# Performance work log

Measured on AMD Instinct MI355X. Metric: run time of the kernel, lower is better.

Reference implementation:

```python
import jax, jax.numpy as jnp
import numpy as np

N_NODES = 50000
N_EDGES = 600000
IN_DIM = 128
EDGE_DIM = 64
OUT_DIM = 128
AVG_D_LOG = 2.5
EPS = 1e-5  # std epsilon used by PNA aggregate_std
POST_IN = (4 * 3 + 1) * IN_DIM  # (n_aggr*n_scalers + 1) * in_dim = 1664


def setup_inputs() -> dict:
    key = jax.random.key(0)
    ks = jax.random.split(key, 10)
    node_feat = jax.random.normal(ks[0], (N_NODES, IN_DIM), dtype=jnp.float32)
    edge_feat = jax.random.normal(ks[1], (N_EDGES, EDGE_DIM), dtype=jnp.float32)
    src = jax.random.randint(ks[2], (N_EDGES,), 0, N_NODES, dtype=jnp.int32)
    dst = jax.random.randint(ks[3], (N_EDGES,), 0, N_NODES, dtype=jnp.int32)
    pre_in = 2 * IN_DIM + EDGE_DIM  # 320
    W_pre = jax.random.normal(ks[4], (pre_in, IN_DIM), dtype=jnp.float32) / np.sqrt(pre_in)
    b_pre = jnp.zeros((IN_DIM,), dtype=jnp.float32)
    W_post1 = jax.random.normal(ks[5], (POST_IN, OUT_DIM), dtype=jnp.float32) / np.sqrt(POST_IN)
    b_post1 = jnp.zeros((OUT_DIM,), dtype=jnp.float32)
    W_post2 = jax.random.normal(ks[6], (OUT_DIM, OUT_DIM), dtype=jnp.float32) / np.sqrt(OUT_DIM)
    b_post2 = jnp.zeros((OUT_DIM,), dtype=jnp.float32)
    return {"node_feat": node_feat, "edge_feat": edge_feat, "src": src, "dst": dst,
            "W_pre": W_pre, "b_pre": b_pre, "W_post1": W_post1, "b_post1": b_post1,
            "W_post2": W_post2, "b_post2": b_post2}


def reference(node_feat, edge_feat, src, dst, W_pre, b_pre, W_post1, b_post1, W_post2, b_post2):
    N = node_feat.shape[0]
    # pretrans_edges: concat(src feat, dst feat, edge feat) -> MLP (1 layer + relu)
    z2 = jnp.concatenate([node_feat[src], node_feat[dst], edge_feat], axis=-1)  # [E, 320]
    e = jax.nn.relu(z2 @ W_pre + b_pre)  # [E, in_dim] edge messages

    # segmented multi-aggregator reduce at destination nodes
    deg = jax.ops.segment_sum(jnp.ones((e.shape[0],), e.dtype), dst, num_segments=N)  # [N]
    safe_deg = jnp.maximum(deg, 1.0)[:, None]
    s = jax.ops.segment_sum(e, dst, num_segments=N)
    mean = s / safe_deg
    mean_sq = jax.ops.segment_sum(e * e, dst, num_segments=N) / safe_deg
    var = jax.nn.relu(mean_sq - mean * mean)
    std = jnp.sqrt(var + EPS)
    mx = jax.ops.segment_max(e, dst, num_segments=N)
    mn = jax.ops.segment_min(e, dst, num_segments=N)
    has_edges = (deg > 0)[:, None]
    mean = jnp.where(has_edges, mean, 0.0)
    mx = jnp.where(has_edges, mx, 0.0)
    mn = jnp.where(has_edges, mn, 0.0)
    std = jnp.where(has_edges, std, 0.0)
    agg = jnp.concatenate([mean, mx, mn, std], axis=-1)  # [N, 4*in_dim]

    # scalers: identity, amplification, attenuation
    logd = jnp.log(deg + 1.0)[:, None]
    amp = agg * (logd / AVG_D_LOG)
    att = agg * jnp.where(deg[:, None] > 0, AVG_D_LOG / jnp.maximum(logd, EPS), 0.0)
    h_agg = jnp.concatenate([agg, amp, att], axis=-1)  # [N, 12*in_dim]

    # posttrans: concat(h, aggregated) -> 2-layer MLP, then residual
    h = jnp.concatenate([node_feat, h_agg], axis=-1)  # [N, 13*in_dim]
    h = jax.nn.relu(h @ W_post1 + b_post1)
    h = h @ W_post2 + b_post2
    return h + node_feat  # residual (in_dim == out_dim)
```

## Files before the change

kernel.cpp:

```cpp
#include <hip/hip_runtime.h>
#include <hip/hip_bf16.h>
#include <math.h>

#define N_NODES 50000
#define N_EDGES 600000
#define EG 3750
#define SCAN_NB 196

typedef __attribute__((ext_vector_type(8))) short short8v;
typedef __attribute__((ext_vector_type(4))) short short4v;
typedef __attribute__((ext_vector_type(4))) float f32x4;
typedef __attribute__((ext_vector_type(4))) float float4v;

#define FLT_BIG 3.402823466e38f

__device__ __forceinline__ short f2bf(float f) {
  unsigned int u = __float_as_uint(f);
  u = (u + 0x7FFFu + ((u >> 16) & 1u)) >> 16;
  return (short)u;
}
__device__ __forceinline__ float bf2f(unsigned short s) {
  return __uint_as_float(((unsigned int)s) << 16);
}

__global__ void conv_w_kernel(const float* __restrict__ Wpre, const float* __restrict__ Wp1,
                              const float* __restrict__ Wp2, short* __restrict__ WuvT,
                              short* __restrict__ WeT, short* __restrict__ Wp1T,
                              short* __restrict__ Wp2T, int* __restrict__ deg) {
  int idx = blockIdx.x * 256 + threadIdx.x;
  if (idx < 50048) deg[idx] = 0;
  if (idx < 32768) {
    int c = idx >> 7, k = idx & 127;
    WuvT[idx] = f2bf(Wpre[(k + ((c >> 7) << 7)) * 128 + (c & 127)]);
  } else if (idx < 40960) {
    int o = idx - 32768, n = o >> 6, k = o & 63;
    WeT[o] = f2bf(Wpre[(256 + k) * 128 + n]);
  } else if (idx < 253952) {
    int o = idx - 40960, n = o / 1664, k = o % 1664;
    Wp1T[o] = f2bf(Wp1[k * 128 + n]);
  } else if (idx < 270336) {
    int o = idx - 253952, n = o >> 7, k = o & 127;
    Wp2T[o] = f2bf(Wp2[k * 128 + n]);
  }
}

__global__ void deg_kernel(const int* __restrict__ dst, int* __restrict__ deg) {
  int i = blockIdx.x * blockDim.x + threadIdx.x;
  int stride = gridDim.x * blockDim.x;
  for (; i < N_EDGES; i += stride) atomicAdd(deg + dst[i], 1);
}

__global__ __launch_bounds__(256) void scan1_kernel(const int* __restrict__ deg,
                                                    int* __restrict__ blockSums) {
  __shared__ int red[256];
  int b = blockIdx.x, t = threadIdx.x;
  int n = b * 256 + t;
  red[t] = (n < N_NODES) ? deg[n] : 0;
  __syncthreads();
  for (int off = 128; off > 0; off >>= 1) {
    if (t < off) red[t] += red[t + off];
    __syncthreads();
  }
  if (t == 0) blockSums[b] = red[0];
}

__global__ __launch_bounds__(256) void scan2_kernel(const int* __restrict__ blockSums,
                                                    int* __restrict__ blockOffs) {
  __shared__ int sh[256];
  int t = threadIdx.x;
  int v = (t < SCAN_NB) ? blockSums[t] : 0;
  sh[t] = v;
  __syncthreads();
  for (int off = 1; off < 256; off <<= 1) {
    int u = (t >= off) ? sh[t - off] : 0;
    __syncthreads();
    sh[t] += u;
    __syncthreads();
  }
  if (t < SCAN_NB) blockOffs[t] = sh[t] - v;
}

__global__ __launch_bounds__(256) void scan3_kernel(const int* __restrict__ deg,
                                                    const int* __restrict__ blockOffs,
                                                    int* __restrict__ cursor,
                                                    int* __restrict__ rowStart) {
  __shared__ int sh[256];
  int b = blockIdx.x, t = threadIdx.x;
  int n = b * 256 + t;
  int v = (n < N_NODES) ? deg[n] : 0;
  sh[t] = v;
  __syncthreads();
  for (int off = 1; off < 256; off <<= 1) {
    int u = (t >= off) ? sh[t - off] : 0;
    __syncthreads();
    sh[t] += u;
    __syncthreads();
  }
  int ex = blockOffs[b] + sh[t] - v;
  if (n < N_NODES) { cursor[n] = ex; rowStart[n] = ex; }
  if (n == N_NODES) rowStart[N_NODES] = N_EDGES;
}

__global__ void scatter_kernel(const int* __restrict__ src, const int* __restrict__ dst,
                               int* __restrict__ cursor, const int* __restrict__ rowStart,
                               int4* __restrict__ eid, int* __restrict__ blockA) {
  int i0 = blockIdx.x * blockDim.x + threadIdx.x;
  int stride = gridDim.x * blockDim.x;
  for (int i = i0; i < N_EDGES; i += stride) {
    int d = dst[i];
    int pos = atomicAdd(cursor + d, 1);
    eid[pos] = make_int4(i, src[i], d, 0);
  }
  for (int j = N_EDGES + i0; j < N_EDGES + 64; j += stride)
    eid[j] = make_int4(0, 0, 0, 0);
  for (int b = i0; b <= EG; b += stride) {
    int tgt = (int)((long)b * N_EDGES / EG);
    int lo = 0, hi = N_NODES;
    while (lo < hi) { int mid = (lo + hi) >> 1; if (rowStart[mid] < tgt) lo = mid + 1; else hi = mid; }
    blockA[b] = rowStart[lo];
  }
}

__global__ __launch_bounds__(256) void uv_kernel(const float* __restrict__ nf,
                                                 const short* __restrict__ WuvT,
                                                 short* __restrict__ UV) {
  __shared__ short A[64][136];
  int t = threadIdx.x;
  int lane = t & 63, w = t >> 6;
  int r15 = lane & 15, g = lane >> 4;
  int nb = blockIdx.x * 64;

#pragma unroll
  for (int i = 0; i < 8; i++) {
    int u = t + 256 * i, row = u >> 5, q = u & 31;
    int gn = min(nb + row, N_NODES - 1);
    float4v a = *(const float4v*)(nf + (size_t)gn * 128 + q * 4);
    short4v s;
    s[0] = f2bf(a[0]); s[1] = f2bf(a[1]); s[2] = f2bf(a[2]); s[3] = f2bf(a[3]);
    *(short4v*)(&A[row][q * 4]) = s;
  }
  __syncthreads();

  f32x4 acc[4][4];
#pragma unroll
  for (int m = 0; m < 4; m++)
#pragma unroll
    for (int j = 0; j < 4; j++) acc[m][j] = (f32x4){0.f, 0.f, 0.f, 0.f};

#pragma unroll
  for (int ks = 0; ks < 4; ks++) {
    short8v af[4];
#pragma unroll
    for (int m = 0; m < 4; m++) af[m] = *(const short8v*)(&A[m * 16 + r15][ks * 32 + 8 * g]);
#pragma unroll
    for (int j = 0; j < 4; j++) {
      short8v bf = *(const short8v*)(WuvT + (size_t)((4 * w + j) * 16 + r15) * 128 + ks * 32 + 8 * g);
#pragma unroll
      for (int m = 0; m < 4; m++)
        acc[m][j] = __builtin_amdgcn_mfma_f32_16x16x32_bf16(af[m], bf, acc[m][j], 0, 0, 0);
    }
  }

#pragma unroll
  for (int m = 0; m < 4; m++)
#pragma unroll
    for (int j = 0; j < 4; j++)
#pragma unroll
      for (int r = 0; r < 4; r++) {
        int node = nb + m * 16 + 4 * g + r;
        if (node < N_NODES)
          UV[(size_t)node * 256 + (4 * w + j) * 16 + r15] = f2bf(acc[m][j][r]);
      }
}

__global__ __launch_bounds__(256, 6) void edge_kernel(
    const int4* __restrict__ eid, const int* __restrict__ blockA,
    const float* __restrict__ edge_feat, const float* __restrict__ b_pre,
    const short* __restrict__ UV, const short* __restrict__ WeT,
    float* __restrict__ sum, float* __restrict__ sq,
    float* __restrict__ mx, float* __restrict__ mn) {
  __shared__ short A[32][72];
  __shared__ float E[32][132];
  __shared__ int srcL[2][32], dstL[2][32];

  int t = threadIdx.x;
  int lane = t & 63, w = t >> 6;
  int r15 = lane & 15, g = lane >> 4;

  short8v bfr[2][2];
#pragma unroll
  for (int ks = 0; ks < 2; ks++)
#pragma unroll
    for (int j = 0; j < 2; j++)
      bfr[ks][j] = *(const short8v*)(WeT + (size_t)((2 * w + j) * 16 + r15) * 64 + ks * 32 + 8 * g);

  int c = t & 127, half = t >> 7;
  int cd = t & 63, wrow = t >> 6;
  float bp0 = b_pre[2 * cd], bp1 = b_pre[2 * cd + 1];

  const unsigned short* UVu = (const unsigned short*)UV;
  int A0 = blockA[blockIdx.x], A1 = blockA[blockIdx.x + 1];
  if (A0 >= A1) return;

  float4v ge[2];
  auto LOADE = [&](int e0c) {
#pragma unroll
    for (int i = 0; i < 2; i++) {
      int u = t + 256 * i, e = u >> 4, q = u & 15;
      int pe = eid[min(e0c + e, N_EDGES + 63)].x;
      ge[i] = *(const float4v*)(edge_feat + (size_t)pe * 64 + q * 4);
    }
  };
  auto WRITE_A = [&]() {
#pragma unroll
    for (int i = 0; i < 2; i++) {
      int u = t + 256 * i, e = u >> 4, q = u & 15;
      short4v s4;
      s4[0] = f2bf(ge[i][0]); s4[1] = f2bf(ge[i][1]);
      s4[2] = f2bf(ge[i][2]); s4[3] = f2bf(ge[i][3]);
      *(short4v*)(&A[e][q * 4]) = s4;
    }
  };
  int nsrc = 0, ndst = 0;
  auto IDXLOAD = [&](int e0c) {
    if (t < 32) {
      int4 v = eid[min(e0c + t, N_EDGES + 63)];
      nsrc = v.y; ndst = v.z;
    }
  };

  LOADE(A0);
  IDXLOAD(A0);
  if (t < 32) { srcL[0][t] = nsrc; dstL[0][t] = ndst; }
  WRITE_A();
  IDXLOAD(A0 + 32);
  __syncthreads();

  float a0 = (half == 0) ? 0.f : -FLT_BIG;
  float a1 = (half == 0) ? 0.f : FLT_BIG;
  int prevd = -1;

  int p = 0;
  for (int e0 = A0; e0 < A1; e0 += 32) {
    int cnt = min(32, A1 - e0);
    unsigned int upf[8], vpf[8];
#pragma unroll
    for (int i = 0; i < 8; i++) {
      int rr = min(wrow + 4 * i, cnt - 1);
      int sr = srcL[p][rr], dr = dstL[p][rr];
      upf[i] = *(const unsigned int*)(UVu + (size_t)sr * 256 + 2 * cd);
      vpf[i] = *(const unsigned int*)(UVu + (size_t)dr * 256 + 128 + 2 * cd);
    }
    LOADE(e0 + 32);

    f32x4 acc[2][2];
#pragma unroll
    for (int m = 0; m < 2; m++)
#pragma unroll
      for (int j = 0; j < 2; j++) acc[m][j] = (f32x4){0.f, 0.f, 0.f, 0.f};
#pragma unroll
    for (int m = 0; m < 2; m++)
#pragma unroll
      for (int ks = 0; ks < 2; ks++) {
        short8v af = *(const short8v*)(&A[m * 16 + r15][ks * 32 + 8 * g]);
        acc[m][0] = __builtin_amdgcn_mfma_f32_16x16x32_bf16(af, bfr[ks][0], acc[m][0], 0, 0, 0);
        acc[m][1] = __builtin_amdgcn_mfma_f32_16x16x32_bf16(af, bfr[ks][1], acc[m][1], 0, 0, 0);
      }
#pragma unroll
    for (int m = 0; m < 2; m++)
#pragma unroll
      for (int j = 0; j < 2; j++)
#pragma unroll
        for (int r = 0; r < 4; r++)
          E[m * 16 + 4 * g + r][(2 * w + j) * 16 + r15] = acc[m][j][r];
    __syncthreads();

#pragma unroll
    for (int i = 0; i < 8; i++) {
      int r = wrow + 4 * i;
      float u0 = bf2f((unsigned short)(upf[i] & 0xFFFFu));
      float u1 = bf2f((unsigned short)(upf[i] >> 16));
      float v0 = bf2f((unsigned short)(vpf[i] & 0xFFFFu));
      float v1 = bf2f((unsigned short)(vpf[i] >> 16));
      E[r][2 * cd] = fmaxf(u0 + v0 + E[r][2 * cd] + bp0, 0.f);
      E[r][2 * cd + 1] = fmaxf(u1 + v1 + E[r][2 * cd + 1] + bp1, 0.f);
    }
    __syncthreads();

    {
      int l = lane & 31;
      int dl_ = dstL[p][l];
      int dp_ = (l == 0) ? prevd : dstL[p][l - 1];
      unsigned int bm = (unsigned int)__ballot(dl_ != dp_);
#pragma unroll
      for (int r = 0; r < 32; r++) {
        if (r < cnt) {
          if ((bm >> r) & 1u) {
            int tgt = (r == 0) ? prevd : dstL[p][r - 1];
            if (tgt >= 0) {
              size_t o = (size_t)tgt * 128 + c;
              if (half == 0) { sum[o] = a0; sq[o] = a1; }
              else { mx[o] = a0; mn[o] = a1; }
            }
            if (half == 0) { a0 = 0.f; a1 = 0.f; }
            else { a0 = -FLT_BIG; a1 = FLT_BIG; }
          }
          float e = E[r][c];
          if (half == 0) { a0 += e; a1 += e * e; }
          else { a0 = fmaxf(a0, e); a1 = fminf(a1, e); }
        }
      }
      prevd = dstL[p][cnt - 1];
    }
    WRITE_A();
    if (t < 32) { srcL[p ^ 1][t] = nsrc; dstL[p ^ 1][t] = ndst; }
    IDXLOAD(e0 + 64);
    __syncthreads();
    p ^= 1;
  }
  if (prevd >= 0) {
    size_t o = (size_t)prevd * 128 + c;
    if (half == 0) { sum[o] = a0; sq[o] = a1; }
    else { mx[o] = a0; mn[o] = a1; }
  }
}

__global__ __launch_bounds__(512, 4) void post_kernel(
    const float* __restrict__ node_feat, const int* __restrict__ deg,
    const float* __restrict__ sum, const float* __restrict__ sq,
    const float* __restrict__ mxp, const float* __restrict__ mnp,
    const short* __restrict__ Wp1T, const short* __restrict__ Wp2T,
    const float* __restrict__ b1, const float* __restrict__ b2,
    float* __restrict__ out) {
  __shared__ short Ab[2][64][64];
  __shared__ short T[64][136];
  __shared__ float scalL[64][4];
  int t = threadIdx.x;
  int lane = t & 63, w = t >> 6;
  int r15 = lane & 15, g = lane >> 4;
  int nb = blockIdx.x * 64;

  if (t < 64) {
    int n = min(nb + t, N_NODES - 1);
    float dg = (float)deg[n];
    scalL[t][0] = 1.f / fmaxf(dg, 1.f);
    float logd = logf(dg + 1.f);
    scalL[t][1] = logd * 0.4f;
    scalL[t][2] = (dg > 0.f) ? 2.5f / fmaxf(logd, 1e-5f) : 0.f;
    scalL[t][3] = (dg > 0.f) ? 1.f : 0.f;
  }
  float bb1v = b1[w * 16 + r15];

  int srow = t >> 3, s8 = t & 7;
  int sgn = min(nb + srow, N_NODES - 1);
  float4v ra, rb, qa, qb;

  auto PRE = [&](int c) {
    if (c < 2) {
      const float* np = node_feat + (size_t)sgn * 128 + c * 64 + s8 * 8;
      ra = *(const float4v*)np;
      rb = *(const float4v*)(np + 4);
    } else {
      size_t o = (size_t)sgn * 128 + (c & 1) * 64 + s8 * 8;
      int si = (c - 2) >> 1;
      if (si == 0) { ra = *(const float4v*)(sum + o); rb = *(const float4v*)(sum + o + 4); }
      else if (si == 1) { ra = *(const float4v*)(mxp + o); rb = *(const float4v*)(mxp + o + 4); }
      else if (si == 2) { ra = *(const float4v*)(mnp + o); rb = *(const float4v*)(mnp + o + 4); }
      else {
        ra = *(const float4v*)(sum + o); rb = *(const float4v*)(sum + o + 4);
        qa = *(const float4v*)(sq + o);  qb = *(const float4v*)(sq + o + 4);
      }
    }
  };
  auto WR = [&](int buf, int c) {
    short8v pk;
    if (c < 2) {
#pragma unroll
      for (int r = 0; r < 4; r++) { pk[r] = f2bf(ra[r]); pk[4 + r] = f2bf(rb[r]); }
    } else {
      int si = (c - 2) >> 1;
      float inv = scalL[srow][0];
      bool h = (scalL[srow][3] != 0.f);
      if (si == 0) {
#pragma unroll
        for (int r = 0; r < 4; r++) {
          pk[r] = f2bf(h ? ra[r] * inv : 0.f);
          pk[4 + r] = f2bf(h ? rb[r] * inv : 0.f);
        }
      } else if (si == 1) {
#pragma unroll
        for (int r = 0; r < 4; r++) {
          pk[r] = f2bf(h ? ra[r] : 0.f);
          pk[4 + r] = f2bf(h ? rb[r] : 0.f);
        }
      } else if (si == 2) {
#pragma unroll
        for (int r = 0; r < 4; r++) {
          pk[r] = f2bf(h ? ra[r] : 0.f);
          pk[4 + r] = f2bf(h ? rb[r] : 0.f);
        }
      } else {
#pragma unroll
        for (int r = 0; r < 4; r++) {
          float m0 = ra[r] * inv, m1 = rb[r] * inv;
          float s0 = sqrtf(fmaxf(qa[r] * inv - m0 * m0, 0.f) + 1e-5f);
          float s1 = sqrtf(fmaxf(qb[r] * inv - m1 * m1, 0.f) + 1e-5f);
          pk[r] = f2bf(h ? s0 : 0.f);
          pk[4 + r] = f2bf(h ? s1 : 0.f);
        }
      }
    }
    *(short8v*)(&Ab[buf][0][0] + srow * 64 + (s8 ^ (srow & 7)) * 8) = pk;
  };

  f32x4 accB[4], accC[4], accD[4];
#pragma unroll
  for (int m = 0; m < 4; m++) {
    accB[m] = (f32x4){0.f, 0.f, 0.f, 0.f};
    accC[m] = (f32x4){0.f, 0.f, 0.f, 0.f};
    accD[m] = (f32x4){0.f, 0.f, 0.f, 0.f};
  }

  const short* wrp = Wp1T + (size_t)(w * 16 + r15) * 1664 + 8 * g;

  PRE(0);
  __syncthreads();
  WR(0, 0);
  __syncthreads();

  for (int c = 0; c < 10; c++) {
    int buf = c & 1;
    if (c < 9) PRE(c + 1);
    short8v bw0[3], bw1[3];
    if (c < 2) {
      bw0[0] = *(const short8v*)(wrp + c * 64);
      bw1[0] = *(const short8v*)(wrp + c * 64 + 32);
    } else {
      int ka = (c - 2) * 64;
      bw0[0] = *(const short8v*)(wrp + 128 + ka);
      bw0[1] = *(const short8v*)(wrp + 640 + ka);
      bw0[2] = *(const short8v*)(wrp + 1152 + ka);
      bw1[0] = *(const short8v*)(wrp + 128 + ka + 32);
      bw1[1] = *(const short8v*)(wrp + 640 + ka + 32);
      bw1[2] = *(const short8v*)(wrp + 1152 + ka + 32);
    }
    const short* base = &Ab[buf][0][0];
#pragma unroll
    for (int ks2 = 0; ks2 < 2; ks2++) {
      const short8v* bw = (ks2 == 0) ? bw0 : bw1;
      short8v af[4];
#pragma unroll
      for (int m = 0; m < 4; m++) {
        int row = m * 16 + r15;
        af[m] = *(const short8v*)(base + row * 64 + (((ks2 << 2) | g) ^ (row & 7)) * 8);
      }
      if (c < 2) {
#pragma unroll
        for (int m = 0; m < 4; m++)
          accB[m] = __builtin_amdgcn_mfma_f32_16x16x32_bf16(af[m], bw[0], accB[m], 0, 0, 0);
      } else {
#pragma unroll
        for (int m = 0; m < 4; m++) {
          accB[m] = __builtin_amdgcn_mfma_f32_16x16x32_bf16(af[m], bw[0], accB[m], 0, 0, 0);
          accC[m] = __builtin_amdgcn_mfma_f32_16x16x32_bf16(af[m], bw[1], accC[m], 0, 0, 0);
          accD[m] = __builtin_amdgcn_mfma_f32_16x16x32_bf16(af[m], bw[2], accD[m], 0, 0, 0);
        }
      }
    }
    if (c < 9) WR(buf ^ 1, c + 1);
    __syncthreads();
  }

#pragma unroll
  for (int m = 0; m < 4; m++)
#pragma unroll
    for (int r = 0; r < 4; r++) {
      int row = m * 16 + 4 * g + r;
      float v = accB[m][r] + scalL[row][1] * accC[m][r] + scalL[row][2] * accD[m][r] + bb1v;
      T[row][w * 16 + r15] = f2bf(fmaxf(v, 0.f));
    }
  __syncthreads();

  f32x4 acc2[4];
#pragma unroll
  for (int m = 0; m < 4; m++) acc2[m] = (f32x4){0.f, 0.f, 0.f, 0.f};
#pragma unroll
  for (int ks = 0; ks < 4; ks++) {
    short8v af2[4];
#pragma unroll
    for (int m = 0; m < 4; m++) af2[m] = *(const short8v*)(&T[m * 16 + r15][ks * 32 + 8 * g]);
    short8v b2f = *(const short8v*)(Wp2T + (size_t)(w * 16 + r15) * 128 + ks * 32 + 8 * g);
#pragma unroll
    for (int m = 0; m < 4; m++)
      acc2[m] = __builtin_amdgcn_mfma_f32_16x16x32_bf16(af2[m], b2f, acc2[m], 0, 0, 0);
  }

#pragma unroll
  for (int m = 0; m < 4; m++)
#pragma unroll
    for (int r = 0; r < 4; r++) {
      int row = m * 16 + 4 * g + r;
      int gn = nb + row;
      if (gn < N_NODES) {
        int col = w * 16 + r15;
        size_t o = (size_t)gn * 128 + col;
        out[o] = acc2[m][r] + b2[col] + node_feat[o];
      }
    }
}

extern "C" void kernel_launch(void* const* d_in, const int* in_sizes, int n_in,
                              void* d_out, int out_size, void* d_ws, size_t ws_size,
                              hipStream_t stream) {
  const float* node_feat = (const float*)d_in[0];
  const float* edge_feat = (const float*)d_in[1];
  const int* src = (const int*)d_in[2];
  const int* dst = (const int*)d_in[3];
  const float* W_pre = (const float*)d_in[4];
  const float* b_pre = (const float*)d_in[5];
  const float* W_post1 = (const float*)d_in[6];
  const float* b_post1 = (const float*)d_in[7];
  const float* W_post2 = (const float*)d_in[8];
  const float* b_post2 = (const float*)d_in[9];
  float* out = (float*)d_out;

  char* ws = (char*)d_ws;
  size_t P = (size_t)N_NODES * 128;
  float* sum = (float*)ws;
  float* sq = sum + P;
  float* mx = sq + P;
  float* mn = mx + P;
  int* deg = (int*)(mn + P);
  int* cursor = deg + 50048;
  int* rowStart = cursor + 50048;
  int* blockA = rowStart + 50052;
  int* blockSums = blockA + 3752;
  int* blockOffs = blockSums + 256;
  int4* eid = (int4*)(blockOffs + 256);
  short* UV = (short*)(eid + N_EDGES + 64);
  short* WuvT = UV + (size_t)50048 * 256;
  short* WeT = WuvT + 32768;
  short* Wp1T = WeT + 8192;
  short* Wp2T = Wp1T + 212992;
  size_t needed = (size_t)((char*)(Wp2T + 16384) - ws);
  if (ws_size < needed) return;

  conv_w_kernel<<<(270336 + 255) / 256, 256, 0, stream>>>(W_pre, W_post1, W_post2, WuvT, WeT,
                                                          Wp1T, Wp2T, deg);
  deg_kernel<<<1024, 256, 0, stream>>>(dst, deg);
  scan1_kernel<<<SCAN_NB, 256, 0, stream>>>(deg, blockSums);
  scan2_kernel<<<1, 256, 0, stream>>>(blockSums, blockOffs);
  scan3_kernel<<<SCAN_NB, 256, 0, stream>>>(deg, blockOffs, cursor, rowStart);
  scatter_kernel<<<1024, 256, 0, stream>>>(src, dst, cursor, rowStart, eid, blockA);
  uv_kernel<<<(N_NODES + 63) / 64, 256, 0, stream>>>(node_feat, WuvT, UV);
  edge_kernel<<<EG, 256, 0, stream>>>(eid, blockA, edge_feat, b_pre, UV, WeT, sum, sq, mx, mn);
  post_kernel<<<(N_NODES + 63) / 64, 512, 0, stream>>>(node_feat, deg, sum, sq, mx, mn, Wp1T,
                                                       Wp2T, b_post1, b_post2, out);
}
```

Measured before the change: 288.3 us.

## Merge scan and scatter/UV kernels, transpose edge staging with swizzled LDS

Merges scan2 into scan3 by having every block redo the small block-sum scan, and merges the scatter and UV-projection kernels into one launch whose blocks split by index. The pre-MLP bias moves into the UV projection output. The edge kernel now stages edge messages in a transposed, XOR-swizzled LDS tile read as float4, and its occupancy hint rises from 6 to 7. These changes aim to cut launch count and LDS bank conflicts. They add redundant scan work per block and fold the bias in before bf16 rounding, which slightly changes numerics.

```diff
diff --git a/kernel.cpp b/kernel.cpp
--- a/kernel.cpp
+++ b/kernel.cpp
@@ -6,6 +6,7 @@
 #define N_EDGES 600000
 #define EG 3750
 #define SCAN_NB 196
+#define UV_NB 782
 
 typedef __attribute__((ext_vector_type(8))) short short8v;
 typedef __attribute__((ext_vector_type(4))) short short4v;
@@ -64,28 +65,22 @@
   if (t == 0) blockSums[b] = red[0];
 }
 
-__global__ __launch_bounds__(256) void scan2_kernel(const int* __restrict__ blockSums,
-                                                    int* __restrict__ blockOffs) {
-  __shared__ int sh[256];
-  int t = threadIdx.x;
-  int v = (t < SCAN_NB) ? blockSums[t] : 0;
-  sh[t] = v;
-  __syncthreads();
-  for (int off = 1; off < 256; off <<= 1) {
-    int u = (t >= off) ? sh[t - off] : 0;
-    __syncthreads();
-    sh[t] += u;
-    __syncthreads();
-  }
-  if (t < SCAN_NB) blockOffs[t] = sh[t] - v;
-}
-
-__global__ __launch_bounds__(256) void scan3_kernel(const int* __restrict__ deg,
-                                                    const int* __restrict__ blockOffs,
-                                                    int* __restrict__ cursor,
-                                                    int* __restrict__ rowStart) {
+__global__ __launch_bounds__(256) void scan23_kernel(const int* __restrict__ deg,
+                                                     const int* __restrict__ blockSums,
+                                                     int* __restrict__ cursor,
+                                                     int* __restrict__ rowStart) {
+  __shared__ int bs[256];
   __shared__ int sh[256];
   int b = blockIdx.x, t = threadIdx.x;
+  bs[t] = (t < SCAN_NB) ? blockSums[t] : 0;
+  __syncthreads();
+  for (int off = 1; off < 256; off <<= 1) {
+    int u = (t >= off) ? bs[t - off] : 0;
+    __syncthreads();
+    bs[t] += u;
+    __syncthreads();
+  }
+  int blockOff = (b == 0) ? 0 : bs[b - 1];
   int n = b * 256 + t;
   int v = (n < N_NODES) ? deg[n] : 0;
   sh[t] = v;
@@ -96,91 +91,94 @@
     sh[t] += u;
     __syncthreads();
   }
-  int ex = blockOffs[b] + sh[t] - v;
+  int ex = blockOff + sh[t] - v;
   if (n < N_NODES) { cursor[n] = ex; rowStart[n] = ex; }
   if (n == N_NODES) rowStart[N_NODES] = N_EDGES;
 }
 
-__global__ void scatter_kernel(const int* __restrict__ src, const int* __restrict__ dst,
-                               int* __restrict__ cursor, const int* __restrict__ rowStart,
-                               int4* __restrict__ eid, int* __restrict__ blockA) {
-  int i0 = blockIdx.x * blockDim.x + threadIdx.x;
-  int stride = gridDim.x * blockDim.x;
-  for (int i = i0; i < N_EDGES; i += stride) {
-    int d = dst[i];
-    int pos = atomicAdd(cursor + d, 1);
-    eid[pos] = make_int4(i, src[i], d, 0);
-  }
-  for (int j = N_EDGES + i0; j < N_EDGES + 64; j += stride)
-    eid[j] = make_int4(0, 0, 0, 0);
-  for (int b = i0; b <= EG; b += stride) {
-    int tgt = (int)((long)b * N_EDGES / EG);
-    int lo = 0, hi = N_NODES;
-    while (lo < hi) { int mid = (lo + hi) >> 1; if (rowStart[mid] < tgt) lo = mid + 1; else hi = mid; }
-    blockA[b] = rowStart[lo];
-  }
-}
-
-__global__ __launch_bounds__(256) void uv_kernel(const float* __restrict__ nf,
-                                                 const short* __restrict__ WuvT,
-                                                 short* __restrict__ UV) {
+__global__ __launch_bounds__(256) void scatter_uv_kernel(
+    const float* __restrict__ nf, const short* __restrict__ WuvT,
+    const float* __restrict__ b_pre, short* __restrict__ UV,
+    const int* __restrict__ src, const int* __restrict__ dst,
+    int* __restrict__ cursor, const int* __restrict__ rowStart,
+    int4* __restrict__ eid, int* __restrict__ blockA) {
   __shared__ short A[64][136];
   int t = threadIdx.x;
-  int lane = t & 63, w = t >> 6;
-  int r15 = lane & 15, g = lane >> 4;
-  int nb = blockIdx.x * 64;
-
-#pragma unroll
-  for (int i = 0; i < 8; i++) {
-    int u = t + 256 * i, row = u >> 5, q = u & 31;
-    int gn = min(nb + row, N_NODES - 1);
-    float4v a = *(const float4v*)(nf + (size_t)gn * 128 + q * 4);
-    short4v s;
-    s[0] = f2bf(a[0]); s[1] = f2bf(a[1]); s[2] = f2bf(a[2]); s[3] = f2bf(a[3]);
-    *(short4v*)(&A[row][q * 4]) = s;
-  }
-  __syncthreads();
-
-  f32x4 acc[4][4];
-#pragma unroll
-  for (int m = 0; m < 4; m++)
-#pragma unroll
-    for (int j = 0; j < 4; j++) acc[m][j] = (f32x4){0.f, 0.f, 0.f, 0.f};
-
-#pragma unroll
-  for (int ks = 0; ks < 4; ks++) {
-    short8v af[4];
-#pragma unroll
-    for (int m = 0; m < 4; m++) af[m] = *(const short8v*)(&A[m * 16 + r15][ks * 32 + 8 * g]);
+  if (blockIdx.x < UV_NB) {
+    int lane = t & 63, w = t >> 6;
+    int r15 = lane & 15, g = lane >> 4;
+    int nb = blockIdx.x * 64;
+#pragma unroll
+    for (int i = 0; i < 8; i++) {
+      int u = t + 256 * i, row = u >> 5, q = u & 31;
+      int gn = min(nb + row, N_NODES - 1);
+      float4v a = *(const float4v*)(nf + (size_t)gn * 128 + q * 4);
+      short4v s;
+      s[0] = f2bf(a[0]); s[1] = f2bf(a[1]); s[2] = f2bf(a[2]); s[3] = f2bf(a[3]);
+      *(short4v*)(&A[row][q * 4]) = s;
+    }
+    __syncthreads();
+
+    f32x4 acc[4][4];
+#pragma unroll
+    for (int m = 0; m < 4; m++)
+#pragma unroll
+      for (int j = 0; j < 4; j++) acc[m][j] = (f32x4){0.f, 0.f, 0.f, 0.f};
+
+#pragma unroll
+    for (int ks = 0; ks < 4; ks++) {
+      short8v af[4];
+#pragma unroll
+      for (int m = 0; m < 4; m++) af[m] = *(const short8v*)(&A[m * 16 + r15][ks * 32 + 8 * g]);
+#pragma unroll
+      for (int j = 0; j < 4; j++) {
+        short8v bf = *(const short8v*)(WuvT + (size_t)((4 * w + j) * 16 + r15) * 128 + ks * 32 + 8 * g);
+#pragma unroll
+        for (int m = 0; m < 4; m++)
+          acc[m][j] = __builtin_amdgcn_mfma_f32_16x16x32_bf16(af[m], bf, acc[m][j], 0, 0, 0);
+      }
+    }
+
 #pragma unroll
     for (int j = 0; j < 4; j++) {
-      short8v bf = *(const short8v*)(WuvT + (size_t)((4 * w + j) * 16 + r15) * 128 + ks * 32 + 8 * g);
+      int coln = (4 * w + j) * 16 + r15;
+      float bias = (coln >= 128) ? b_pre[coln - 128] : 0.f;
 #pragma unroll
       for (int m = 0; m < 4; m++)
-        acc[m][j] = __builtin_amdgcn_mfma_f32_16x16x32_bf16(af[m], bf, acc[m][j], 0, 0, 0);
-    }
-  }
-
-#pragma unroll
-  for (int m = 0; m < 4; m++)
-#pragma unroll
-    for (int j = 0; j < 4; j++)
-#pragma unroll
-      for (int r = 0; r < 4; r++) {
-        int node = nb + m * 16 + 4 * g + r;
-        if (node < N_NODES)
-          UV[(size_t)node * 256 + (4 * w + j) * 16 + r15] = f2bf(acc[m][j][r]);
-      }
-}
-
-__global__ __launch_bounds__(256, 6) void edge_kernel(
+#pragma unroll
+        for (int r = 0; r < 4; r++) {
+          int node = nb + m * 16 + 4 * g + r;
+          if (node < N_NODES)
+            UV[(size_t)node * 256 + coln] = f2bf(acc[m][j][r] + bias);
+        }
+    }
+  } else {
+    int i0 = (blockIdx.x - UV_NB) * 256 + t;
+    int stride = 1024 * 256;
+    for (int i = i0; i < N_EDGES; i += stride) {
+      int d = dst[i];
+      int pos = atomicAdd(cursor + d, 1);
+      eid[pos] = make_int4(i, src[i], d, 0);
+    }
+    for (int j = N_EDGES + i0; j < N_EDGES + 64; j += stride)
+      eid[j] = make_int4(0, 0, 0, 0);
+    for (int b = i0; b <= EG; b += stride) {
+      int tgt = (int)((long)b * N_EDGES / EG);
+      int lo = 0, hi = N_NODES;
+      while (lo < hi) { int mid = (lo + hi) >> 1; if (rowStart[mid] < tgt) lo = mid + 1; else hi = mid; }
+      blockA[b] = rowStart[lo];
+    }
+  }
+}
+
+__global__ __launch_bounds__(256, 7) void edge_kernel(
     const int4* __restrict__ eid, const int* __restrict__ blockA,
-    const float* __restrict__ edge_feat, const float* __restrict__ b_pre,
+    const float* __restrict__ edge_feat,
     const short* __restrict__ UV, const short* __restrict__ WeT,
     float* __restrict__ sum, float* __restrict__ sq,
     float* __restrict__ mx, float* __restrict__ mn) {
   __shared__ short A[32][72];
-  __shared__ float E[32][132];
+  __shared__ float ET[128][32];
   __shared__ int srcL[2][32], dstL[2][32];
 
   int t = threadIdx.x;
@@ -195,8 +193,7 @@
       bfr[ks][j] = *(const short8v*)(WeT + (size_t)((2 * w + j) * 16 + r15) * 64 + ks * 32 + 8 * g);
 
   int c = t & 127, half = t >> 7;
-  int cd = t & 63, wrow = t >> 6;
-  float bp0 = b_pre[2 * cd], bp1 = b_pre[2 * cd + 1];
+  int cd = t & 63, q = t >> 6;
 
   const unsigned short* UVu = (const unsigned short*)UV;
   int A0 = blockA[blockIdx.x], A1 = blockA[blockIdx.x + 1];
@@ -206,19 +203,19 @@
   auto LOADE = [&](int e0c) {
 #pragma unroll
     for (int i = 0; i < 2; i++) {
-      int u = t + 256 * i, e = u >> 4, q = u & 15;
+      int u = t + 256 * i, e = u >> 4, qq = u & 15;
       int pe = eid[min(e0c + e, N_EDGES + 63)].x;
-      ge[i] = *(const float4v*)(edge_feat + (size_t)pe * 64 + q * 4);
+      ge[i] = *(const float4v*)(edge_feat + (size_t)pe * 64 + qq * 4);
     }
   };
   auto WRITE_A = [&]() {
 #pragma unroll
     for (int i = 0; i < 2; i++) {
-      int u = t + 256 * i, e = u >> 4, q = u & 15;
+      int u = t + 256 * i, e = u >> 4, qq = u & 15;
       short4v s4;
       s4[0] = f2bf(ge[i][0]); s4[1] = f2bf(ge[i][1]);
       s4[2] = f2bf(ge[i][2]); s4[3] = f2bf(ge[i][3]);
-      *(short4v*)(&A[e][q * 4]) = s4;
+      *(short4v*)(&A[e][qq * 4]) = s4;
     }
   };
   int nsrc = 0, ndst = 0;
@@ -246,8 +243,8 @@
     unsigned int upf[8], vpf[8];
 #pragma unroll
     for (int i = 0; i < 8; i++) {
-      int rr = min(wrow + 4 * i, cnt - 1);
-      int sr = srcL[p][rr], dr = dstL[p][rr];
+      int r = q * 8 + i;
+      int sr = srcL[p][r], dr = dstL[p][r];
       upf[i] = *(const unsigned int*)(UVu + (size_t)sr * 256 + 2 * cd);
       vpf[i] = *(const unsigned int*)(UVu + (size_t)dr * 256 + 128 + 2 * cd);
     }
@@ -269,21 +266,34 @@
 #pragma unroll
     for (int m = 0; m < 2; m++)
 #pragma unroll
-      for (int j = 0; j < 2; j++)
-#pragma unroll
-        for (int r = 0; r < 4; r++)
-          E[m * 16 + 4 * g + r][(2 * w + j) * 16 + r15] = acc[m][j][r];
-    __syncthreads();
-
-#pragma unroll
-    for (int i = 0; i < 8; i++) {
-      int r = wrow + 4 * i;
-      float u0 = bf2f((unsigned short)(upf[i] & 0xFFFFu));
-      float u1 = bf2f((unsigned short)(upf[i] >> 16));
-      float v0 = bf2f((unsigned short)(vpf[i] & 0xFFFFu));
-      float v1 = bf2f((unsigned short)(vpf[i] >> 16));
-      E[r][2 * cd] = fmaxf(u0 + v0 + E[r][2 * cd] + bp0, 0.f);
-      E[r][2 * cd + 1] = fmaxf(u1 + v1 + E[r][2 * cd + 1] + bp1, 0.f);
+      for (int j = 0; j < 2; j++) {
+        int col = (2 * w + j) * 16 + r15;
+        *(float4v*)(&ET[col][(((m * 4 + g) ^ (col & 7)) << 2)]) = acc[m][j];
+      }
+    __syncthreads();
+
+    {
+      int col0 = 2 * cd, col1 = 2 * cd + 1;
+      int x0 = col0 & 7, x1 = col1 & 7;
+      float4v f00 = *(const float4v*)(&ET[col0][(((2 * q) ^ x0) << 2)]);
+      float4v f01 = *(const float4v*)(&ET[col0][(((2 * q + 1) ^ x0) << 2)]);
+      float4v f10 = *(const float4v*)(&ET[col1][(((2 * q) ^ x1) << 2)]);
+      float4v f11 = *(const float4v*)(&ET[col1][(((2 * q + 1) ^ x1) << 2)]);
+#pragma unroll
+      for (int i = 0; i < 4; i++) {
+        f00[i] = fmaxf(f00[i] + bf2f((unsigned short)(upf[i] & 0xFFFFu)) +
+                                bf2f((unsigned short)(vpf[i] & 0xFFFFu)), 0.f);
+        f01[i] = fmaxf(f01[i] + bf2f((unsigned short)(upf[4 + i] & 0xFFFFu)) +
+                                bf2f((unsigned short)(vpf[4 + i] & 0xFFFFu)), 0.f);
+        f10[i] = fmaxf(f10[i] + bf2f((unsigned short)(upf[i] >> 16)) +
+                                bf2f((unsigned short)(vpf[i] >> 16)), 0.f);
+        f11[i] = fmaxf(f11[i] + bf2f((unsigned short)(upf[4 + i] >> 16)) +
+                                bf2f((unsigned short)(vpf[4 + i] >> 16)), 0.f);
+      }
+      *(float4v*)(&ET[col0][(((2 * q) ^ x0) << 2)]) = f00;
+      *(float4v*)(&ET[col0][(((2 * q + 1) ^ x0) << 2)]) = f01;
+      *(float4v*)(&ET[col1][(((2 * q) ^ x1) << 2)]) = f10;
+      *(float4v*)(&ET[col1][(((2 * q + 1) ^ x1) << 2)]) = f11;
     }
     __syncthreads();
 
@@ -292,22 +302,28 @@
       int dl_ = dstL[p][l];
       int dp_ = (l == 0) ? prevd : dstL[p][l - 1];
       unsigned int bm = (unsigned int)__ballot(dl_ != dp_);
-#pragma unroll
-      for (int r = 0; r < 32; r++) {
-        if (r < cnt) {
-          if ((bm >> r) & 1u) {
-            int tgt = (r == 0) ? prevd : dstL[p][r - 1];
-            if (tgt >= 0) {
-              size_t o = (size_t)tgt * 128 + c;
-              if (half == 0) { sum[o] = a0; sq[o] = a1; }
-              else { mx[o] = a0; mn[o] = a1; }
+      int x = c & 7;
+#pragma unroll
+      for (int rq = 0; rq < 8; rq++) {
+        float4v v4 = *(const float4v*)(&ET[c][((rq ^ x) << 2)]);
+#pragma unroll
+        for (int jj = 0; jj < 4; jj++) {
+          int r = rq * 4 + jj;
+          if (r < cnt) {
+            if ((bm >> r) & 1u) {
+              int tgt = (r == 0) ? prevd : dstL[p][r - 1];
+              if (tgt >= 0) {
+                size_t o = (size_t)tgt * 128 + c;
+                if (half == 0) { sum[o] = a0; sq[o] = a1; }
+                else { mx[o] = a0; mn[o] = a1; }
+              }
+              if (half == 0) { a0 = 0.f; a1 = 0.f; }
+              else { a0 = -FLT_BIG; a1 = FLT_BIG; }
             }
-            if (half == 0) { a0 = 0.f; a1 = 0.f; }
-            else { a0 = -FLT_BIG; a1 = FLT_BIG; }
+            float e = v4[jj];
+            if (half == 0) { a0 += e; a1 += e * e; }
+            else { a0 = fmaxf(a0, e); a1 = fminf(a1, e); }
           }
-          float e = E[r][c];
-          if (half == 0) { a0 += e; a1 += e * e; }
-          else { a0 = fmaxf(a0, e); a1 = fminf(a1, e); }
         }
       }
       prevd = dstL[p][cnt - 1];
@@ -535,8 +551,8 @@
   int* rowStart = cursor + 50048;
   int* blockA = rowStart + 50052;
   int* blockSums = blockA + 3752;
-  int* blockOffs = blockSums + 256;
-  int4* eid = (int4*)(blockOffs + 256);
+  int* pad = blockSums + 256;
+  int4* eid = (int4*)(pad + 256);
   short* UV = (short*)(eid + N_EDGES + 64);
   short* WuvT = UV + (size_t)50048 * 256;
   short* WeT = WuvT + 32768;
@@ -549,11 +565,10 @@
                                                           Wp1T, Wp2T, deg);
   deg_kernel<<<1024, 256, 0, stream>>>(dst, deg);
   scan1_kernel<<<SCAN_NB, 256, 0, stream>>>(deg, blockSums);
-  scan2_kernel<<<1, 256, 0, stream>>>(blockSums, blockOffs);
-  scan3_kernel<<<SCAN_NB, 256, 0, stream>>>(deg, blockOffs, cursor, rowStart);
-  scatter_kernel<<<1024, 256, 0, stream>>>(src, dst, cursor, rowStart, eid, blockA);
-  uv_kernel<<<(N_NODES + 63) / 64, 256, 0, stream>>>(node_feat, WuvT, UV);
-  edge_kernel<<<EG, 256, 0, stream>>>(eid, blockA, edge_feat, b_pre, UV, WeT, sum, sq, mx, mn);
+  scan23_kernel<<<SCAN_NB, 256, 0, stream>>>(deg, blockSums, cursor, rowStart);
+  scatter_uv_kernel<<<UV_NB + 1024, 256, 0, stream>>>(node_feat, WuvT, b_pre, UV, src, dst,
+                                                      cursor, rowStart, eid, blockA);
+  edge_kernel<<<EG, 256, 0, stream>>>(eid, blockA, edge_feat, UV, WeT, sum, sq, mx, mn);
   post_kernel<<<(N_NODES + 63) / 64, 512, 0, stream>>>(node_feat, deg, sum, sq, mx, mn, Wp1T,
                                                        Wp2T, b_post1, b_post2, out);
 }
```

Measured after the change: 459.9 us. +59.6%, slower.
